# Performance work log

Measured on AMD Instinct MI355X. Metric: run time of the kernel, lower is better.

The kernel has to match this reference:

```python
import jax, jax.numpy as jnp
import numpy as np

Q_HEADS, KV_HEADS, HEAD_DIM, WINDOW = 16, 4, 128, 512
HIDDEN = 2048
ROPE_BASE = 10000.0


def _rope_tables(T, head_dim, dtype):
    half = head_dim // 2
    inv_freq = 1.0 / (ROPE_BASE ** (jnp.arange(half, dtype=jnp.float32) / half))
    t = jnp.arange(T, dtype=jnp.float32)
    freqs = jnp.outer(t, inv_freq)  # [T, half]
    return jnp.cos(freqs).astype(dtype), jnp.sin(freqs).astype(dtype)


def _apply_rope(x, cos, sin):
    # x: [B, T, H, D]; cos/sin: [T, D//2] -> broadcast [1, T, 1, D//2]
    c = cos[None, :, None, :]
    s = sin[None, :, None, :]
    x1, x2 = jnp.split(x, 2, axis=-1)
    return jnp.concatenate([x1 * c - x2 * s, x1 * s + x2 * c], axis=-1)


def setup_inputs() -> dict:
    key = jax.random.key(0)
    ks = jax.random.split(key, 5)
    B, T = 1, 4096
    x = jax.random.normal(ks[0], (B, T, HIDDEN), dtype=jnp.float32)
    sc = 0.02
    wq = jax.random.normal(ks[1], (Q_HEADS * HEAD_DIM, HIDDEN), dtype=jnp.float32) * sc
    wk = jax.random.normal(ks[2], (KV_HEADS * HEAD_DIM, HIDDEN), dtype=jnp.float32) * sc
    wv = jax.random.normal(ks[3], (KV_HEADS * HEAD_DIM, HIDDEN), dtype=jnp.float32) * sc
    wo = jax.random.normal(ks[4], (HIDDEN, Q_HEADS * HEAD_DIM), dtype=jnp.float32) * sc
    return {"x": x, "wq": wq, "wk": wk, "wv": wv, "wo": wo}


def reference(x, wq, wk, wv, wo):
    B, T, _ = x.shape
    reps = Q_HEADS // KV_HEADS
    scale = 1.0 / np.sqrt(HEAD_DIM)

    q = jnp.einsum('bth,oh->bto', x, wq).reshape(B, T, Q_HEADS, HEAD_DIM)
    k = jnp.einsum('bth,oh->bto', x, wk).reshape(B, T, KV_HEADS, HEAD_DIM)
    v = jnp.einsum('bth,oh->bto', x, wv).reshape(B, T, KV_HEADS, HEAD_DIM)

    cos, sin = _rope_tables(T, HEAD_DIM, x.dtype)
    q = _apply_rope(q, cos, sin)
    k = _apply_rope(k, cos, sin)

    # GQA without materializing repeated K/V: group q as [B,T,KVH,reps,D]
    qg = q.reshape(B, T, KV_HEADS, reps, HEAD_DIM)
    scores = jnp.einsum('btgrd,bsgd->bgrts', qg, k) * scale  # [B,KVH,reps,T,T]

    idx = jnp.arange(T)
    # allowed: causal (s <= t) AND within window (t - s <= WINDOW)
    allowed = (idx[None, :] <= idx[:, None]) & (idx[:, None] - idx[None, :] <= WINDOW)
    scores = jnp.where(allowed[None, None, None], scores, jnp.finfo(scores.dtype).min)
    probs = jax.nn.softmax(scores, axis=-1)

    out = jnp.einsum('bgrts,bsgd->btgrd', probs, v)  # [B,T,KVH,reps,D]
    out = out.reshape(B, T, Q_HEADS * HEAD_DIM)
    return jnp.einsum('bto,ho->bth', out, wo)
```

## Files before the change

### kernel.cpp

```cpp
#include <hip/hip_runtime.h>

typedef __attribute__((ext_vector_type(8))) short short8;
typedef __attribute__((ext_vector_type(4))) float f32x4;
typedef __attribute__((ext_vector_type(4))) unsigned short u16x4;

__device__ __forceinline__ unsigned short f2b(float f) {
  unsigned int u = __float_as_uint(f);
  u += 0x7fffu + ((u >> 16) & 1u);
  return (unsigned short)(u >> 16);
}
__device__ __forceinline__ void glds16(const void* g, void* l) {
  __builtin_amdgcn_global_load_lds(
      (const __attribute__((address_space(1))) unsigned int*)g,
      (__attribute__((address_space(3))) unsigned int*)l, 16, 0, 0);
}

__global__ __launch_bounds__(256) void cast_all(const float* __restrict__ x,
                                                const float* __restrict__ wq,
                                                const float* __restrict__ wk,
                                                const float* __restrict__ wv,
                                                const float* __restrict__ wo,
                                                unsigned short* __restrict__ dst) {
  const int i = blockIdx.x * 256 + threadIdx.x;
  const float* s;
  int off;
  if (i < 2097152)      { s = x;  off = i; }
  else if (i < 3145728) { s = wq; off = i - 2097152; }
  else if (i < 3407872) { s = wk; off = i - 3145728; }
  else if (i < 3670016) { s = wv; off = i - 3407872; }
  else                  { s = wo; off = i - 3670016; }
  f32x4 v = ((const f32x4*)s)[off];
  u16x4 o;
  o[0] = f2b(v[0]); o[1] = f2b(v[1]); o[2] = f2b(v[2]); o[3] = f2b(v[3]);
  ((u16x4*)dst)[i] = o;
}

__global__ __launch_bounds__(512, 2) void gemm256(
    const unsigned short* __restrict__ A, const unsigned short* __restrict__ B,
    const int Karg, const int mode,
    unsigned short* __restrict__ qb, unsigned short* __restrict__ kb,
    unsigned short* __restrict__ vtg, float* __restrict__ Cout, const int Narg) {
  extern __shared__ char smem[];
  const int tid = threadIdx.x;
  const int w = tid >> 6, lane = tid & 63;
  const int quad = lane >> 4, l15 = lane & 15;
  const int wm = w >> 2, wn = w & 3;
  const int m0 = blockIdx.x * 256, n0 = blockIdx.y * 256;

  int nb[4];
#pragma unroll
  for (int ni = 0; ni < 4; ++ni) {
    const int bbi = (wn & 1) * 4 + ni;
    nb[ni] = mode ? ((bbi & 1) ? 4 + (bbi >> 1) : (bbi >> 1)) : bbi;
  }

  const int fragOff = l15 * 64 + ((quad * 16) ^ ((l15 & 8) << 2));
  char* const aWave = smem + wm * 16384;
  char* const bWave = smem + 32768 + (wn >> 1) * 16384;

  const int sr = lane >> 2;
  const int sc = ((lane & 3) * 8) ^ ((lane & 32) ? 16 : 0);
  const unsigned short* const Abase = A + (size_t)(m0 + (w >> 1) * 16 + sr) * 2048 + (w & 1) * 32 + sc;
  const unsigned short* const Bbase = B + (size_t)(n0 + (w >> 1) * 16 + sr) * 2048 + (w & 1) * 32 + sc;

#define BARF()                            \
  asm volatile("" ::: "memory");          \
  __builtin_amdgcn_s_barrier();           \
  asm volatile("" ::: "memory");

#define STAGE_AJ(h, tt, jj)                                                              \
  {                                                                                      \
    const int t_ = ((tt) < 32) ? (tt) : 31;                                              \
    glds16(Abase + (size_t)(h) * (128 * 2048) + (jj) * (64 * 2048) + (size_t)t_ * 64,    \
           smem + (t_ & 1) * 65536 + (h) * 16384 + (jj) * 8192 + w * 1024);              \
  }
#define STAGE_B2(h, tt)                                                                  \
  {                                                                                      \
    const int t_ = ((tt) < 32) ? (tt) : 31;                                              \
    char* const d_ = smem + (t_ & 1) * 65536 + 32768 + (h) * 16384 + w * 1024;           \
    glds16(Bbase + (size_t)(h) * (128 * 2048) + (size_t)t_ * 64, d_);                    \
    glds16(Bbase + (size_t)(h) * (128 * 2048) + (64 * 2048) + (size_t)t_ * 64, d_ + 8192); \
  }
#define RD_A(dst, c, MI0)                                                                \
  _Pragma("unroll") for (int mi = 0; mi < 4; ++mi)                                       \
  _Pragma("unroll") for (int kk = 0; kk < 2; ++kk)                                       \
      dst[mi][kk] = *(const short8*)(aWave + (c) * 65536 + (((MI0) + mi) * 2 + kk) * 1024 + fragOff);
#define RD_B(dst, c, NI0)                                                                \
  _Pragma("unroll") for (int ni = 0; ni < 2; ++ni)                                       \
  _Pragma("unroll") for (int kk = 0; kk < 2; ++kk)                                       \
      dst[ni][kk] = *(const short8*)(bWave + (c) * 65536 + (nb[(NI0) + ni] * 2 + kk) * 1024 + fragOff);

  f32x4 acc[8][4];
  const f32x4 fz = {0.f, 0.f, 0.f, 0.f};
#pragma unroll
  for (int i = 0; i < 8; ++i)
#pragma unroll
    for (int j = 0; j < 4; ++j) acc[i][j] = fz;

  short8 af[4][2], blo[2][2], bhi[2][2];

#define MFMA_Q(MOFF, NOFF, BF)                                                   \
  _Pragma("unroll") for (int kk = 0; kk < 2; ++kk)                               \
  _Pragma("unroll") for (int mi = 0; mi < 4; ++mi)                               \
  _Pragma("unroll") for (int ni = 0; ni < 2; ++ni)                               \
      acc[(MOFF) + mi][(NOFF) + ni] = __builtin_amdgcn_mfma_f32_16x16x32_bf16(   \
          af[mi][kk], BF[ni][kk], acc[(MOFF) + mi][(NOFF) + ni], 0, 0, 0);

  STAGE_AJ(0, 0, 0) STAGE_AJ(1, 0, 0) STAGE_B2(0, 0) STAGE_B2(1, 0) STAGE_AJ(0, 0, 1) STAGE_AJ(1, 0, 1)
  STAGE_AJ(0, 1, 0) STAGE_AJ(1, 1, 0) STAGE_B2(0, 1) STAGE_B2(1, 1) STAGE_AJ(0, 1, 1) STAGE_AJ(1, 1, 1)
  asm volatile("s_waitcnt vmcnt(8)" ::: "memory");
  BARF()

#define TILE(c, tt)                                                                  \
   asm volatile("s_waitcnt vmcnt(8)" ::: "memory");                          \
  RD_A(af, (c), 0) RD_B(blo, (c), 0)                                                 \
  BARF()                                                                             \
  __builtin_amdgcn_s_setprio(1); MFMA_Q(0, 0, blo) __builtin_amdgcn_s_setprio(0);    \
  BARF()                                                                             \
   RD_B(bhi, (c), 2)                                                         \
  STAGE_AJ(0, (tt) + 2, 0) STAGE_AJ(1, (tt) + 2, 0)                                  \
  BARF()                                                                             \
  __builtin_amdgcn_s_setprio(1); MFMA_Q(0, 2, bhi) __builtin_amdgcn_s_setprio(0);    \
  BARF()                                                                             \
   RD_A(af, (c), 4)                                                          \
  STAGE_B2(0, (tt) + 2) STAGE_B2(1, (tt) + 2)                                        \
  BARF()                                                                             \
  __builtin_amdgcn_s_setprio(1); MFMA_Q(4, 2, bhi) __builtin_amdgcn_s_setprio(0);    \
  BARF()                                                                             \
   STAGE_AJ(0, (tt) + 2, 1) STAGE_AJ(1, (tt) + 2, 1)                         \
  BARF()                                                                             \
  __builtin_amdgcn_s_setprio(1); MFMA_Q(4, 0, blo) __builtin_amdgcn_s_setprio(0);    \
  BARF()

#pragma unroll 1
  for (int T = 0; T < 32; T += 2) {
    TILE(0, T)
    TILE(1, T + 1)
  }
  asm volatile("s_waitcnt vmcnt(0)" ::: "memory");
#undef TILE
#undef MFMA_Q
#undef RD_A
#undef RD_B
#undef STAGE_AJ
#undef STAGE_B2
#undef BARF

  if (mode == 0) {
    const int colBase = n0 + wn * 64;
#pragma unroll
    for (int mi = 0; mi < 8; ++mi) {
      const int row = m0 + wm * 128 + mi * 16 + quad * 4;
#pragma unroll
      for (int ni = 0; ni < 4; ++ni) {
        const int col = colBase + ni * 16 + l15;
#pragma unroll
        for (int r = 0; r < 4; ++r)
          Cout[(size_t)(row + r) * 2048 + col] = acc[mi][ni][r];
      }
    }
    return;
  }

  const int y = blockIdx.y;
  const int tb0 = m0 + wm * 128;
  if (y >= 10) {
    const int g = (y - 10) * 2 + (wn >> 1);
#pragma unroll
    for (int mi = 0; mi < 8; ++mi) {
      const int tb = tb0 + mi * 16 + quad * 4;
#pragma unroll
      for (int ni = 0; ni < 4; ++ni) {
        const int d = nb[ni] * 16 + l15;
        u16x4 o;
#pragma unroll
        for (int r = 0; r < 4; ++r) o[r] = f2b(acc[mi][ni][r]);
        *(u16x4*)(vtg + (size_t)(g * 128 + d) * 4096 + tb) = o;
      }
    }
  } else {
    unsigned short* dst;
    int stride, hoff;
    if (y < 8) { dst = qb; stride = 2048; hoff = (y * 2 + (wn >> 1)) * 128; }
    else       { dst = kb; stride = 512;  hoff = ((y - 8) * 2 + (wn >> 1)) * 128; }
    const float c2 = 0.20762050593045889f;
    const float inv2pi = 0.15915494309189535f;
#pragma unroll
    for (int j = 0; j < 2; ++j) {
      const int i = ((wn & 1) * 2 + j) * 16 + l15;
      const float inv_rev = exp2f(-(float)i * c2) * inv2pi;
#pragma unroll
      for (int mi = 0; mi < 8; ++mi) {
#pragma unroll
        for (int r = 0; r < 4; ++r) {
          const int t = tb0 + mi * 16 + quad * 4 + r;
          float rev = (float)t * inv_rev;
          rev -= floorf(rev);
          const float sn = __builtin_amdgcn_sinf(rev);
          const float cs = __builtin_amdgcn_cosf(rev);
          const float x1 = acc[mi][2 * j][r], x2 = acc[mi][2 * j + 1][r];
          unsigned short* p = dst + (size_t)t * stride + hoff + i;
          p[0]  = f2b(x1 * cs - x2 * sn);
          p[64] = f2b(x1 * sn + x2 * cs);
        }
      }
    }
  }
}

__global__ __launch_bounds__(512, 2) void gemm128(const unsigned short* __restrict__ A,
                                                  const unsigned short* __restrict__ B,
                                                  float* __restrict__ Cout) {
  extern __shared__ char smem[];
  const int tid = threadIdx.x;
  const int w = tid >> 6, lane = tid & 63;
  const int quad = lane >> 4, l15 = lane & 15;
  const int wm = w >> 2, wn = w & 3;
  const int m0 = blockIdx.x * 128, n0 = blockIdx.y * 256;

  const int fragOff = l15 * 64 + ((quad * 16) ^ ((l15 & 8) << 2));
  char* const aWave = smem;
  char* const bWave = smem + 16384 + (wn >> 1) * 16384;

  const int sr = lane >> 2;
  const int sc = ((lane & 3) * 8) ^ ((lane & 32) ? 16 : 0);
  const unsigned short* const Abase = A + (size_t)(m0 + (w >> 1) * 16 + sr) * 2048 + (w & 1) * 32 + sc;
  const unsigned short* const Bbase = B + (size_t)(n0 + (w >> 1) * 16 + sr) * 2048 + (w & 1) * 32 + sc;

#define BARF()                            \
  asm volatile("" ::: "memory");          \
  __builtin_amdgcn_s_barrier();           \
  asm volatile("" ::: "memory");

#define G_STAGE_A(tt)                                                                    \
  {                                                                                      \
    const int t_ = ((tt) < 32) ? (tt) : 31;                                              \
    char* const d_ = smem + (t_ & 1) * 49152 + w * 1024;                                 \
    glds16(Abase + (size_t)t_ * 64, d_);                                                 \
    glds16(Abase + (64 * 2048) + (size_t)t_ * 64, d_ + 8192);                            \
  }
#define G_STAGE_B(h, tt)                                                                 \
  {                                                                                      \
    const int t_ = ((tt) < 32) ? (tt) : 31;                                              \
    char* const d_ = smem + (t_ & 1) * 49152 + 16384 + (h) * 16384 + w * 1024;           \
    glds16(Bbase + (size_t)(h) * (128 * 2048) + (size_t)t_ * 64, d_);                    \
    glds16(Bbase + (size_t)(h) * (128 * 2048) + (64 * 2048) + (size_t)t_ * 64, d_ + 8192); \
  }
#define G_RD_A(c)                                                                        \
  _Pragma("unroll") for (int mi = 0; mi < 4; ++mi)                                       \
  _Pragma("unroll") for (int kk = 0; kk < 2; ++kk)                                       \
      af[mi][kk] = *(const short8*)(aWave + (c) * 49152 + ((wm * 4 + mi) * 2 + kk) * 1024 + fragOff);
#define G_RD_B(dst, c, NI0)                                                              \
  _Pragma("unroll") for (int ni = 0; ni < 2; ++ni)                                       \
  _Pragma("unroll") for (int kk = 0; kk < 2; ++kk)                                       \
      dst[ni][kk] = *(const short8*)(bWave + (c) * 49152 + (((wn & 1) * 4 + (NI0) + ni) * 2 + kk) * 1024 + fragOff);

  f32x4 acc[4][4];
  const f32x4 fz = {0.f, 0.f, 0.f, 0.f};
#pragma unroll
  for (int i = 0; i < 4; ++i)
#pragma unroll
    for (int j = 0; j < 4; ++j) acc[i][j] = fz;

  short8 af[4][2], blo[2][2], bhi[2][2];

#define G_MFMA(NOFF, BF)                                                         \
  _Pragma("unroll") for (int kk = 0; kk < 2; ++kk)                               \
  _Pragma("unroll") for (int mi = 0; mi < 4; ++mi)                               \
  _Pragma("unroll") for (int ni = 0; ni < 2; ++ni)                               \
      acc[mi][(NOFF) + ni] = __builtin_amdgcn_mfma_f32_16x16x32_bf16(            \
          af[mi][kk], BF[ni][kk], acc[mi][(NOFF) + ni], 0, 0, 0);

  G_STAGE_A(0) G_STAGE_B(0, 0) G_STAGE_B(1, 0) G_STAGE_A(1)
  asm volatile("s_waitcnt vmcnt(2)" ::: "memory");
  BARF()

#define G_TILE(c, tt)                                                                \
   asm volatile("s_waitcnt vmcnt(2)" ::: "memory");                          \
  G_RD_A(c) G_RD_B(blo, (c), 0)                                                      \
  G_STAGE_B(0, (tt) + 1) G_STAGE_B(1, (tt) + 1)                                      \
  BARF()                                                                             \
  __builtin_amdgcn_s_setprio(1); G_MFMA(0, blo) __builtin_amdgcn_s_setprio(0);       \
  BARF()                                                                             \
   G_RD_B(bhi, (c), 2)                                                       \
  G_STAGE_A((tt) + 2)                                                                \
  BARF()                                                                             \
  __builtin_amdgcn_s_setprio(1); G_MFMA(2, bhi) __builtin_amdgcn_s_setprio(0);       \
  BARF()

#pragma unroll 1
  for (int T = 0; T < 32; T += 2) {
    G_TILE(0, T)
    G_TILE(1, T + 1)
  }
  asm volatile("s_waitcnt vmcnt(0)" ::: "memory");
#undef G_TILE
#undef G_MFMA
#undef G_RD_A
#undef G_RD_B
#undef G_STAGE_A
#undef G_STAGE_B
#undef BARF

  const int colBase = n0 + wn * 64;
#pragma unroll
  for (int mi = 0; mi < 4; ++mi) {
    const int row = m0 + wm * 64 + mi * 16 + quad * 4;
#pragma unroll
    for (int ni = 0; ni < 4; ++ni) {
      const int col = colBase + ni * 16 + l15;
#pragma unroll
      for (int r = 0; r < 4; ++r)
        Cout[(size_t)(row + r) * 2048 + col] = acc[mi][ni][r];
    }
  }
}

__global__ __launch_bounds__(512) void attn_fwd(const unsigned short* __restrict__ qp,
                                                const unsigned short* __restrict__ kp,
                                                const unsigned short* __restrict__ vtg,
                                                unsigned short* __restrict__ op) {
  __shared__ unsigned short Ks[2][4][1024];
  __shared__ unsigned short Vt[2][4096];
  const int tid = threadIdx.x;
  const int w = tid >> 6, lane = tid & 63;
  const int quad = lane >> 4, l15 = lane & 15;
  const int t0 = blockIdx.x * 64;
  const int g = blockIdx.y;
  const int h = g * 4 + (w & 3);
  const int t0w = t0 + (w >> 2) * 32;
  const f32x4 fzero = {0.f, 0.f, 0.f, 0.f};
  const float scale = 0.088388347648318447f;
  const float NEG_INF = -__builtin_inff();

  short8 qf[4][2];
#pragma unroll
  for (int qt = 0; qt < 2; qt++) {
    const unsigned short* qrow = qp + (size_t)(t0w + qt * 16 + l15) * 2048 + h * 128 + quad * 8;
#pragma unroll
    for (int kb = 0; kb < 4; kb++) qf[kb][qt] = *(const short8*)(qrow + kb * 32);
  }

  f32x4 oacc[8][2];
#pragma unroll
  for (int db = 0; db < 8; db++) { oacc[db][0] = fzero; oacc[db][1] = fzero; }
  float Mrow[2] = {-1.0e30f, -1.0e30f}, Lrow[2] = {0.f, 0.f};

  const int s_begin = (t0 >= 512) ? (t0 - 512) : 0;
  const int nch = ((t0 + 63 - s_begin) >> 5) + 1;

  const int r4 = lane >> 2, c4 = lane & 3;
#define ATTN_STAGE(s0_, b_)                                                              \
  {                                                                                      \
    const int s0v = (s0_);                                                               \
    if (w < 4) {                                                                         \
      _Pragma("unroll")                                                                  \
      for (int p = 0; p < 2; p++)                                                        \
        glds16(kp + (size_t)(s0v + p * 16 + r4) * 512 + g * 128 + w * 32 + c4 * 8,       \
               &Ks[b_][w][p * 512]);                                                     \
    } else {                                                                             \
      const int wv = w - 4;                                                              \
      _Pragma("unroll")                                                                  \
      for (int p = 0; p < 2; p++)                                                        \
        glds16(vtg + (size_t)(g * 128 + wv * 32 + p * 16 + r4) * 4096 + s0v + c4 * 8,    \
               &Vt[b_][wv * 1024 + p * 512]);                                            \
    }                                                                                    \
  }

  ATTN_STAGE(s_begin, 0);

  for (int c = 0; c < nch; ++c) {
    const int s0 = s_begin + c * 32;
    const int b = c & 1;
    __syncthreads();
    if (c + 1 < nch) ATTN_STAGE(s_begin + (c + 1) * 32, (c + 1) & 1);

    if (s0 + 31 >= t0w - 512 && s0 <= t0w + 31) {
      f32x4 sacc[2][2];
      sacc[0][0] = fzero; sacc[0][1] = fzero; sacc[1][0] = fzero; sacc[1][1] = fzero;
      const int permBase = ((l15 >> 2) << 3) + (l15 & 3);
#pragma unroll
      for (int kb = 0; kb < 4; kb++) {
        short8 af0 = *(const short8*)&Ks[b][kb][(permBase + 0) * 32 + quad * 8];
        short8 af1 = *(const short8*)&Ks[b][kb][(permBase + 4) * 32 + quad * 8];
        sacc[0][0] = __builtin_amdgcn_mfma_f32_16x16x32_bf16(af0, qf[kb][0], sacc[0][0], 0, 0, 0);
        sacc[0][1] = __builtin_amdgcn_mfma_f32_16x16x32_bf16(af0, qf[kb][1], sacc[0][1], 0, 0, 0);
        sacc[1][0] = __builtin_amdgcn_mfma_f32_16x16x32_bf16(af1, qf[kb][0], sacc[1][0], 0, 0, 0);
        sacc[1][1] = __builtin_amdgcn_mfma_f32_16x16x32_bf16(af1, qf[kb][1], sacc[1][1], 0, 0, 0);
      }

      short8 pb[2];
      float alpha[2];
#pragma unroll
      for (int qt = 0; qt < 2; qt++) {
        const int tq = t0w + qt * 16 + l15;
        float vals[8];
        float cmax = NEG_INF;
#pragma unroll
        for (int kt = 0; kt < 2; kt++)
#pragma unroll
          for (int r = 0; r < 4; r++) {
            const int s = s0 + quad * 8 + kt * 4 + r;
            const bool ok = (unsigned)(tq - s) <= 512u;
            const float v = ok ? sacc[kt][qt][r] * scale : NEG_INF;
            vals[kt * 4 + r] = v;
            cmax = fmaxf(cmax, v);
          }
        cmax = fmaxf(cmax, __shfl_xor(cmax, 16));
        cmax = fmaxf(cmax, __shfl_xor(cmax, 32));
        const float Mnew = fmaxf(Mrow[qt], cmax);
        alpha[qt] = __expf(Mrow[qt] - Mnew);
        Mrow[qt] = Mnew;
        float csum = 0.f;
#pragma unroll
        for (int j = 0; j < 8; j++) {
          const float p = __expf(vals[j] - Mnew);
          csum += p;
          pb[qt][j] = (short)f2b(p);
        }
        csum += __shfl_xor(csum, 16);
        csum += __shfl_xor(csum, 32);
        Lrow[qt] = Lrow[qt] * alpha[qt] + csum;
      }

#pragma unroll
      for (int db = 0; db < 8; db++) {
        short8 vf = *(const short8*)&Vt[b][(db * 16 + l15) * 32 + quad * 8];
#pragma unroll
        for (int qt = 0; qt < 2; qt++) {
          oacc[db][qt][0] *= alpha[qt]; oacc[db][qt][1] *= alpha[qt];
          oacc[db][qt][2] *= alpha[qt]; oacc[db][qt][3] *= alpha[qt];
          oacc[db][qt] = __builtin_amdgcn_mfma_f32_16x16x32_bf16(vf, pb[qt], oacc[db][qt], 0, 0, 0);
        }
      }
    }
  }
#undef ATTN_STAGE

#pragma unroll
  for (int qt = 0; qt < 2; qt++) {
    const float invL = 1.f / Lrow[qt];
    unsigned short* orow = op + (size_t)(t0w + qt * 16 + l15) * 2048 + h * 128;
#pragma unroll
    for (int db = 0; db < 8; db++) {
      u16x4 o;
#pragma unroll
      for (int r = 0; r < 4; r++) o[r] = f2b(oacc[db][qt][r] * invL);
      *(u16x4*)(orow + db * 16 + quad * 4) = o;
    }
  }
}

extern "C" void kernel_launch(void* const* d_in, const int* in_sizes, int n_in,
                              void* d_out, int out_size, void* d_ws, size_t ws_size,
                              hipStream_t stream) {
  const float* x  = (const float*)d_in[0];
  const float* wq = (const float*)d_in[1];
  const float* wk = (const float*)d_in[2];
  const float* wv = (const float*)d_in[3];
  const float* wo = (const float*)d_in[4];
  float* out = (float*)d_out;
  char* ws = (char*)d_ws;

  unsigned short* xb    = (unsigned short*)(ws + 0);
  unsigned short* wqkv  = (unsigned short*)(ws + 16777216);
  unsigned short* wob   = (unsigned short*)(ws + 29360128);
  unsigned short* qb    = (unsigned short*)(ws + 37748736);
  unsigned short* kbuf  = (unsigned short*)(ws + 54525952);
  unsigned short* vtg   = (unsigned short*)(ws + 58720256);
  unsigned short* attnb = xb;

  static bool attr_done = false;
  if (!attr_done) {
    hipFuncSetAttribute(reinterpret_cast<const void*>(gemm256),
                        hipFuncAttributeMaxDynamicSharedMemorySize, 131072);
    hipFuncSetAttribute(reinterpret_cast<const void*>(gemm128),
                        hipFuncAttributeMaxDynamicSharedMemorySize, 98304);
    attr_done = true;
  }

  cast_all<<<18432, 256, 0, stream>>>(x, wq, wk, wv, wo, (unsigned short*)ws);

  gemm256<<<dim3(16, 12), 512, 131072, stream>>>(xb, wqkv, 2048, 1,
                                                 qb, kbuf, vtg, nullptr, 0);

  attn_fwd<<<dim3(64, 4), 512, 0, stream>>>(qb, kbuf, vtg, attnb);

  gemm128<<<dim3(32, 8), 512, 98304, stream>>>(attnb, wob, out);
}
```

Measured before the change: 244.6 us.

## Replace 256x256 QKV GEMM with 128x128-tile kernel for more blocks

The fused QKV projection kernel moves from 256x256 output tiles (192 blocks, 128KB LDS, 2 blocks/CU) to 128x128 tiles (768 blocks, 64KB LDS, up to 4 blocks/CU). The staging, fragment reads and RoPE/V-transpose epilogue are reworked for the smaller tile, and the vmcnt wait moves to the end of each tile in both GEMMs. The aim is better CU fill and latency hiding on 256 CUs, since 192 blocks underfill the device. The cost is less operand reuse per block and more global and LDS traffic.

```diff
diff --git a/kernel.cpp b/kernel.cpp
--- a/kernel.cpp
+++ b/kernel.cpp
@@ -35,125 +35,116 @@
   ((u16x4*)dst)[i] = o;
 }
 
-__global__ __launch_bounds__(512, 2) void gemm256(
+#define BARF()                            \
+  asm volatile("" ::: "memory");          \
+  __builtin_amdgcn_s_barrier();           \
+  asm volatile("" ::: "memory");
+
+__global__ __launch_bounds__(512, 4) void gemm_t128(
     const unsigned short* __restrict__ A, const unsigned short* __restrict__ B,
-    const int Karg, const int mode,
+    const int mode,
     unsigned short* __restrict__ qb, unsigned short* __restrict__ kb,
-    unsigned short* __restrict__ vtg, float* __restrict__ Cout, const int Narg) {
+    unsigned short* __restrict__ vtg, float* __restrict__ Cout) {
   extern __shared__ char smem[];
   const int tid = threadIdx.x;
   const int w = tid >> 6, lane = tid & 63;
   const int quad = lane >> 4, l15 = lane & 15;
   const int wm = w >> 2, wn = w & 3;
-  const int m0 = blockIdx.x * 256, n0 = blockIdx.y * 256;
-
-  int nb[4];
-#pragma unroll
-  for (int ni = 0; ni < 4; ++ni) {
-    const int bbi = (wn & 1) * 4 + ni;
-    nb[ni] = mode ? ((bbi & 1) ? 4 + (bbi >> 1) : (bbi >> 1)) : bbi;
-  }
+  const int m0 = blockIdx.x * 128;
+  const int y  = blockIdx.y;
+  const int n0 = y * 128;
+
+  int cb[2];
+  cb[0] = mode ? wn : wn * 2;
+  cb[1] = mode ? wn + 4 : wn * 2 + 1;
 
   const int fragOff = l15 * 64 + ((quad * 16) ^ ((l15 & 8) << 2));
-  char* const aWave = smem + wm * 16384;
-  char* const bWave = smem + 32768 + (wn >> 1) * 16384;
-
   const int sr = lane >> 2;
   const int sc = ((lane & 3) * 8) ^ ((lane & 32) ? 16 : 0);
   const unsigned short* const Abase = A + (size_t)(m0 + (w >> 1) * 16 + sr) * 2048 + (w & 1) * 32 + sc;
   const unsigned short* const Bbase = B + (size_t)(n0 + (w >> 1) * 16 + sr) * 2048 + (w & 1) * 32 + sc;
 
-#define BARF()                            \
-  asm volatile("" ::: "memory");          \
-  __builtin_amdgcn_s_barrier();           \
-  asm volatile("" ::: "memory");
-
-#define STAGE_AJ(h, tt, jj)                                                              \
+#define T_STAGE_A(tt)                                                                    \
   {                                                                                      \
     const int t_ = ((tt) < 32) ? (tt) : 31;                                              \
-    glds16(Abase + (size_t)(h) * (128 * 2048) + (jj) * (64 * 2048) + (size_t)t_ * 64,    \
-           smem + (t_ & 1) * 65536 + (h) * 16384 + (jj) * 8192 + w * 1024);              \
-  }
-#define STAGE_B2(h, tt)                                                                  \
+    char* const d_ = smem + (t_ & 1) * 32768 + w * 1024;                                 \
+    glds16(Abase + (size_t)t_ * 64, d_);                                                 \
+    glds16(Abase + (64 * 2048) + (size_t)t_ * 64, d_ + 8192);                            \
+  }
+#define T_STAGE_B(tt)                                                                    \
   {                                                                                      \
     const int t_ = ((tt) < 32) ? (tt) : 31;                                              \
-    char* const d_ = smem + (t_ & 1) * 65536 + 32768 + (h) * 16384 + w * 1024;           \
-    glds16(Bbase + (size_t)(h) * (128 * 2048) + (size_t)t_ * 64, d_);                    \
-    glds16(Bbase + (size_t)(h) * (128 * 2048) + (64 * 2048) + (size_t)t_ * 64, d_ + 8192); \
-  }
-#define RD_A(dst, c, MI0)                                                                \
-  _Pragma("unroll") for (int mi = 0; mi < 4; ++mi)                                       \
+    char* const d_ = smem + (t_ & 1) * 32768 + 16384 + w * 1024;                         \
+    glds16(Bbase + (size_t)t_ * 64, d_);                                                 \
+    glds16(Bbase + (64 * 2048) + (size_t)t_ * 64, d_ + 8192);                            \
+  }
+#define T_RD_AHI(c)                                                                      \
+  _Pragma("unroll") for (int mi = 2; mi < 4; ++mi)                                       \
   _Pragma("unroll") for (int kk = 0; kk < 2; ++kk)                                       \
-      dst[mi][kk] = *(const short8*)(aWave + (c) * 65536 + (((MI0) + mi) * 2 + kk) * 1024 + fragOff);
-#define RD_B(dst, c, NI0)                                                                \
+      af[mi][kk] = *(const short8*)(smem + (c) * 32768 + ((wm * 4 + mi) * 2 + kk) * 1024 + fragOff);
+#define T_RD_ALO(c)                                                                      \
+  _Pragma("unroll") for (int mi = 0; mi < 2; ++mi)                                       \
+  _Pragma("unroll") for (int kk = 0; kk < 2; ++kk)                                       \
+      af[mi][kk] = *(const short8*)(smem + (c) * 32768 + ((wm * 4 + mi) * 2 + kk) * 1024 + fragOff);
+#define T_RD_B(c)                                                                        \
   _Pragma("unroll") for (int ni = 0; ni < 2; ++ni)                                       \
   _Pragma("unroll") for (int kk = 0; kk < 2; ++kk)                                       \
-      dst[ni][kk] = *(const short8*)(bWave + (c) * 65536 + (nb[(NI0) + ni] * 2 + kk) * 1024 + fragOff);
-
-  f32x4 acc[8][4];
+      bf[ni][kk] = *(const short8*)(smem + (c) * 32768 + 16384 + (cb[ni] * 2 + kk) * 1024 + fragOff);
+
+  f32x4 acc[4][2];
   const f32x4 fz = {0.f, 0.f, 0.f, 0.f};
 #pragma unroll
-  for (int i = 0; i < 8; ++i)
-#pragma unroll
-    for (int j = 0; j < 4; ++j) acc[i][j] = fz;
-
-  short8 af[4][2], blo[2][2], bhi[2][2];
-
-#define MFMA_Q(MOFF, NOFF, BF)                                                   \
+  for (int i = 0; i < 4; ++i) { acc[i][0] = fz; acc[i][1] = fz; }
+
+  short8 af[4][2], bf[2][2];
+
+#define T_MFMA(MI0)                                                              \
   _Pragma("unroll") for (int kk = 0; kk < 2; ++kk)                               \
-  _Pragma("unroll") for (int mi = 0; mi < 4; ++mi)                               \
+  _Pragma("unroll") for (int mi = 0; mi < 2; ++mi)                               \
   _Pragma("unroll") for (int ni = 0; ni < 2; ++ni)                               \
-      acc[(MOFF) + mi][(NOFF) + ni] = __builtin_amdgcn_mfma_f32_16x16x32_bf16(   \
-          af[mi][kk], BF[ni][kk], acc[(MOFF) + mi][(NOFF) + ni], 0, 0, 0);
-
-  STAGE_AJ(0, 0, 0) STAGE_AJ(1, 0, 0) STAGE_B2(0, 0) STAGE_B2(1, 0) STAGE_AJ(0, 0, 1) STAGE_AJ(1, 0, 1)
-  STAGE_AJ(0, 1, 0) STAGE_AJ(1, 1, 0) STAGE_B2(0, 1) STAGE_B2(1, 1) STAGE_AJ(0, 1, 1) STAGE_AJ(1, 1, 1)
-  asm volatile("s_waitcnt vmcnt(8)" ::: "memory");
+      acc[(MI0) + mi][ni] = __builtin_amdgcn_mfma_f32_16x16x32_bf16(             \
+          af[(MI0) + mi][kk], bf[ni][kk], acc[(MI0) + mi][ni], 0, 0, 0);
+
+  T_STAGE_A(0) T_STAGE_B(0) T_STAGE_A(1)
+  asm volatile("s_waitcnt vmcnt(2)" ::: "memory");
   BARF()
 
-#define TILE(c, tt)                                                                  \
-   asm volatile("s_waitcnt vmcnt(8)" ::: "memory");                          \
-  RD_A(af, (c), 0) RD_B(blo, (c), 0)                                                 \
-  BARF()                                                                             \
-  __builtin_amdgcn_s_setprio(1); MFMA_Q(0, 0, blo) __builtin_amdgcn_s_setprio(0);    \
-  BARF()                                                                             \
-   RD_B(bhi, (c), 2)                                                         \
-  STAGE_AJ(0, (tt) + 2, 0) STAGE_AJ(1, (tt) + 2, 0)                                  \
-  BARF()                                                                             \
-  __builtin_amdgcn_s_setprio(1); MFMA_Q(0, 2, bhi) __builtin_amdgcn_s_setprio(0);    \
-  BARF()                                                                             \
-   RD_A(af, (c), 4)                                                          \
-  STAGE_B2(0, (tt) + 2) STAGE_B2(1, (tt) + 2)                                        \
-  BARF()                                                                             \
-  __builtin_amdgcn_s_setprio(1); MFMA_Q(4, 2, bhi) __builtin_amdgcn_s_setprio(0);    \
-  BARF()                                                                             \
-   STAGE_AJ(0, (tt) + 2, 1) STAGE_AJ(1, (tt) + 2, 1)                         \
-  BARF()                                                                             \
-  __builtin_amdgcn_s_setprio(1); MFMA_Q(4, 0, blo) __builtin_amdgcn_s_setprio(0);    \
+#define T_TILE(c, tt)                                                                \
+   T_RD_AHI(c)                                                               \
+  asm volatile("" ::: "memory");                                                     \
+  T_RD_ALO(c) T_RD_B(c)                                                              \
+  T_STAGE_B((tt) + 1)                                                                \
+  BARF()                                                                             \
+  __builtin_amdgcn_s_setprio(1); T_MFMA(0) __builtin_amdgcn_s_setprio(0);            \
+  BARF()                                                                             \
+   T_STAGE_A((tt) + 2)                                                       \
+  BARF()                                                                             \
+  __builtin_amdgcn_s_setprio(1); T_MFMA(2) __builtin_amdgcn_s_setprio(0);            \
+  asm volatile("s_waitcnt vmcnt(2)" ::: "memory");                                   \
   BARF()
 
 #pragma unroll 1
   for (int T = 0; T < 32; T += 2) {
-    TILE(0, T)
-    TILE(1, T + 1)
+    T_TILE(0, T)
+    T_TILE(1, T + 1)
   }
   asm volatile("s_waitcnt vmcnt(0)" ::: "memory");
-#undef TILE
-#undef MFMA_Q
-#undef RD_A
-#undef RD_B
-#undef STAGE_AJ
-#undef STAGE_B2
-#undef BARF
-
+#undef T_TILE
+#undef T_MFMA
+#undef T_RD_AHI
+#undef T_RD_ALO
+#undef T_RD_B
+#undef T_STAGE_A
+#undef T_STAGE_B
+
+  const int tb0 = m0 + wm * 64;
   if (mode == 0) {
-    const int colBase = n0 + wn * 64;
-#pragma unroll
-    for (int mi = 0; mi < 8; ++mi) {
-      const int row = m0 + wm * 128 + mi * 16 + quad * 4;
-#pragma unroll
-      for (int ni = 0; ni < 4; ++ni) {
-        const int col = colBase + ni * 16 + l15;
+#pragma unroll
+    for (int mi = 0; mi < 4; ++mi) {
+      const int row = tb0 + mi * 16 + quad * 4;
+#pragma unroll
+      for (int ni = 0; ni < 2; ++ni) {
+        const int col = n0 + cb[ni] * 16 + l15;
 #pragma unroll
         for (int r = 0; r < 4; ++r)
           Cout[(size_t)(row + r) * 2048 + col] = acc[mi][ni][r];
@@ -161,17 +152,14 @@
     }
     return;
   }
-
-  const int y = blockIdx.y;
-  const int tb0 = m0 + wm * 128;
-  if (y >= 10) {
-    const int g = (y - 10) * 2 + (wn >> 1);
-#pragma unroll
-    for (int mi = 0; mi < 8; ++mi) {
+  if (y >= 20) {
+    const int g = y - 20;
+#pragma unroll
+    for (int mi = 0; mi < 4; ++mi) {
       const int tb = tb0 + mi * 16 + quad * 4;
 #pragma unroll
-      for (int ni = 0; ni < 4; ++ni) {
-        const int d = nb[ni] * 16 + l15;
+      for (int ni = 0; ni < 2; ++ni) {
+        const int d = cb[ni] * 16 + l15;
         u16x4 o;
 #pragma unroll
         for (int r = 0; r < 4; ++r) o[r] = f2b(acc[mi][ni][r]);
@@ -181,28 +169,25 @@
   } else {
     unsigned short* dst;
     int stride, hoff;
-    if (y < 8) { dst = qb; stride = 2048; hoff = (y * 2 + (wn >> 1)) * 128; }
-    else       { dst = kb; stride = 512;  hoff = ((y - 8) * 2 + (wn >> 1)) * 128; }
+    if (y < 16) { dst = qb; stride = 2048; hoff = y * 128; }
+    else        { dst = kb; stride = 512;  hoff = (y - 16) * 128; }
     const float c2 = 0.20762050593045889f;
     const float inv2pi = 0.15915494309189535f;
-#pragma unroll
-    for (int j = 0; j < 2; ++j) {
-      const int i = ((wn & 1) * 2 + j) * 16 + l15;
-      const float inv_rev = exp2f(-(float)i * c2) * inv2pi;
-#pragma unroll
-      for (int mi = 0; mi < 8; ++mi) {
-#pragma unroll
-        for (int r = 0; r < 4; ++r) {
-          const int t = tb0 + mi * 16 + quad * 4 + r;
-          float rev = (float)t * inv_rev;
-          rev -= floorf(rev);
-          const float sn = __builtin_amdgcn_sinf(rev);
-          const float cs = __builtin_amdgcn_cosf(rev);
-          const float x1 = acc[mi][2 * j][r], x2 = acc[mi][2 * j + 1][r];
-          unsigned short* p = dst + (size_t)t * stride + hoff + i;
-          p[0]  = f2b(x1 * cs - x2 * sn);
-          p[64] = f2b(x1 * sn + x2 * cs);
-        }
+    const int i = wn * 16 + l15;
+    const float inv_rev = exp2f(-(float)i * c2) * inv2pi;
+#pragma unroll
+    for (int mi = 0; mi < 4; ++mi) {
+#pragma unroll
+      for (int r = 0; r < 4; ++r) {
+        const int t = tb0 + mi * 16 + quad * 4 + r;
+        float rev = (float)t * inv_rev;
+        rev -= floorf(rev);
+        const float sn = __builtin_amdgcn_sinf(rev);
+        const float cs = __builtin_amdgcn_cosf(rev);
+        const float x1 = acc[mi][0][r], x2 = acc[mi][1][r];
+        unsigned short* p = dst + (size_t)t * stride + hoff + i;
+        p[0]  = f2b(x1 * cs - x2 * sn);
+        p[64] = f2b(x1 * sn + x2 * cs);
       }
     }
   }
@@ -227,11 +212,6 @@
   const unsigned short* const Abase = A + (size_t)(m0 + (w >> 1) * 16 + sr) * 2048 + (w & 1) * 32 + sc;
   const unsigned short* const Bbase = B + (size_t)(n0 + (w >> 1) * 16 + sr) * 2048 + (w & 1) * 32 + sc;
 
-#define BARF()                            \
-  asm volatile("" ::: "memory");          \
-  __builtin_amdgcn_s_barrier();           \
-  asm volatile("" ::: "memory");
-
 #define G_STAGE_A(tt)                                                                    \
   {                                                                                      \
     const int t_ = ((tt) < 32) ? (tt) : 31;                                              \
@@ -276,8 +256,7 @@
   BARF()
 
 #define G_TILE(c, tt)                                                                \
-   asm volatile("s_waitcnt vmcnt(2)" ::: "memory");                          \
-  G_RD_A(c) G_RD_B(blo, (c), 0)                                                      \
+   G_RD_A(c) G_RD_B(blo, (c), 0)                                             \
   G_STAGE_B(0, (tt) + 1) G_STAGE_B(1, (tt) + 1)                                      \
   BARF()                                                                             \
   __builtin_amdgcn_s_setprio(1); G_MFMA(0, blo) __builtin_amdgcn_s_setprio(0);       \
@@ -286,6 +265,7 @@
   G_STAGE_A((tt) + 2)                                                                \
   BARF()                                                                             \
   __builtin_amdgcn_s_setprio(1); G_MFMA(2, bhi) __builtin_amdgcn_s_setprio(0);       \
+  asm volatile("s_waitcnt vmcnt(2)" ::: "memory");                                   \
   BARF()
 
 #pragma unroll 1
@@ -300,7 +280,6 @@
 #undef G_RD_B
 #undef G_STAGE_A
 #undef G_STAGE_B
-#undef BARF
 
   const int colBase = n0 + wn * 64;
 #pragma unroll
@@ -472,8 +451,8 @@
 
   static bool attr_done = false;
   if (!attr_done) {
-    hipFuncSetAttribute(reinterpret_cast<const void*>(gemm256),
-                        hipFuncAttributeMaxDynamicSharedMemorySize, 131072);
+    hipFuncSetAttribute(reinterpret_cast<const void*>(gemm_t128),
+                        hipFuncAttributeMaxDynamicSharedMemorySize, 65536);
     hipFuncSetAttribute(reinterpret_cast<const void*>(gemm128),
                         hipFuncAttributeMaxDynamicSharedMemorySize, 98304);
     attr_done = true;
@@ -481,8 +460,7 @@
 
   cast_all<<<18432, 256, 0, stream>>>(x, wq, wk, wv, wo, (unsigned short*)ws);
 
-  gemm256<<<dim3(16, 12), 512, 131072, stream>>>(xb, wqkv, 2048, 1,
-                                                 qb, kbuf, vtg, nullptr, 0);
+  gemm_t128<<<dim3(32, 24), 512, 65536, stream>>>(xb, wqkv, 1, qb, kbuf, vtg, nullptr);
 
   attn_fwd<<<dim3(64, 4), 512, 0, stream>>>(qb, kbuf, vtg, attnb);
 
```

Result: faster. 238.8 us (-2.3%).
